# Kernel optimization log

Measured on AMD Instinct MI355X. Metric: run time of the kernel, lower is better.

Reference implementation:

```python
import jax, jax.numpy as jnp
import numpy as np

N, E = 50000, 800000          # nodes, edges
IN_DIM, HID, OUT = 200, 256, 64  # hidden_dims
R = 2                          # num_relations
NEG_SLOPE = 0.2                # RGATConv default negative_slope
EPS = 1e-16                    # PyG softmax denominator eps


def _glorot(key, shape, fan):
    return jax.random.normal(key, shape, dtype=jnp.float32) / np.float32(np.sqrt(fan))


def setup_inputs() -> dict:
    key = jax.random.key(0)
    ks = jax.random.split(key, 13)
    features = jax.random.normal(ks[0], (N, IN_DIM), dtype=jnp.float32)
    edge_index = jax.random.randint(ks[1], (2, E), 0, N, dtype=jnp.int64)
    edge_type = jax.random.randint(ks[2], (E,), 0, R, dtype=jnp.int64)
    return {
        "features": features,
        "edge_index": edge_index,
        "edge_type": edge_type,
        # RGATConv layer 1 (heads=1, dim=1): weight [R, in, out], q/k [out, 1]
        "w1": _glorot(ks[3], (R, IN_DIM, HID), IN_DIM),
        "q1": _glorot(ks[4], (HID, 1), HID),
        "k1": _glorot(ks[5], (HID, 1), HID),
        # RGATConv layer 2
        "w2": _glorot(ks[6], (R, HID, OUT), HID),
        "q2": _glorot(ks[7], (OUT, 1), OUT),
        "k2": _glorot(ks[8], (OUT, 1), OUT),
        # decoder: Linear(OUT->HID) then Linear(HID->IN_DIM), stored as [in, out]
        "dW1": _glorot(ks[9], (OUT, HID), OUT),
        "db1": jnp.zeros((HID,), jnp.float32),
        "dW2": _glorot(ks[10], (HID, IN_DIM), HID),
        "db2": jnp.zeros((IN_DIM,), jnp.float32),
    }


def rgat_conv(x, src, dst, etype, w, q, k):
    """PyG RGATConv: additive-self-attention, across-relation softmax,
    heads=1, dim=1, concat=False, bias=False, aggr=add (eval mode: no dropout)."""
    n = x.shape[0]
    # relation-specific transform at node level (per-edge bmm factors through nodes)
    xw = jnp.einsum('ni,ric->rnc', x, w)          # [R, N, C]
    qn = jnp.einsum('rnc,ch->rnh', xw, q)         # [R, N, 1]
    kn = jnp.einsum('rnc,ch->rnh', xw, k)         # [R, N, 1]
    # per-edge attention logit: leaky_relu(q_i + k_j)
    alpha = jax.nn.leaky_relu(qn[etype, dst] + kn[etype, src], NEG_SLOPE)  # [E, 1]
    # segment softmax over destination nodes (across relations)
    m = jax.lax.stop_gradient(jax.ops.segment_max(alpha, dst, num_segments=n))
    m = jnp.where(jnp.isfinite(m), m, jnp.float32(0.0))
    ea = jnp.exp(alpha - m[dst])
    denom = jax.ops.segment_sum(ea, dst, num_segments=n)
    att = ea / (denom[dst] + EPS)                 # [E, 1]
    # scatter-add weighted messages
    msg = att * xw[etype, src]                    # [E, C]
    return jax.ops.segment_sum(msg, dst, num_segments=n)  # [N, C]


def reference(features, edge_index, edge_type, w1, q1, k1, w2, q2, k2, dW1, db1, dW2, db2):
    src, dst = edge_index[0], edge_index[1]
    h1 = jax.nn.elu(rgat_conv(features, src, dst, edge_type, w1, q1, k1))
    h2 = jax.nn.elu(rgat_conv(h1, src, dst, edge_type, w2, q2, k2))
    h3 = (h2 @ dW1 + db1) @ dW2 + db2   # decoder (PCA mode: no ReLU)
    return (h2, h3)
```

## Files before the change

kernel.cpp:

```cpp
#include <hip/hip_runtime.h>

#define IN_DIM 200
#define HID    256
#define OUT_D  64
#define RREL   2
#define NEG_SLOPE 0.2f
#define NNODE  50000
#define MPAD   50048

typedef __attribute__((ext_vector_type(8))) short bf16x8;
typedef __attribute__((ext_vector_type(4))) float f32x4;
typedef __attribute__((ext_vector_type(4))) unsigned int u32x4;

__device__ __forceinline__ float bf2f(unsigned short u) {
    union { unsigned int i; float f; } v; v.i = ((unsigned int)u) << 16; return v.f;
}
__device__ __forceinline__ unsigned short f2bf(float f) {
    union { float f; unsigned int i; } v; v.f = f;
    unsigned int u = v.i;
    return (unsigned short)((u + 0x7FFFu + ((u >> 16) & 1u)) >> 16);
}
__device__ __forceinline__ float elu(float v) { return v > 0.f ? v : (__expf(v) - 1.0f); }

__global__ void feat_cvt(const float* __restrict__ in, unsigned short* __restrict__ out, int n)
{
    int t = blockIdx.x * 256 + threadIdx.x;
    int row = t / 50, c4 = (t % 50) * 4;
    if (row >= n) return;
    float4 f = *(const float4*)(in + (long long)row * 200 + c4);
    *(ushort4*)(out + (long long)row * 200 + c4) =
        make_ushort4(f2bf(f.x), f2bf(f.y), f2bf(f.z), f2bf(f.w));
}

__global__ void wt_cvt(const float* __restrict__ in, unsigned short* __restrict__ out,
                       int Kreal, int Nreal, int Kpad, int Npad, int nb)
{
    long long total = (long long)nb * Npad * Kpad;
    long long idx = (long long)blockIdx.x * 256 + threadIdx.x;
    if (idx >= total) return;
    int kk = (int)(idx % Kpad);
    long long t = idx / Kpad;
    int nrow = (int)(t % Npad);
    int z = (int)(t / Npad);
    float f = (kk < Kreal && nrow < Nreal) ? in[((long long)z * Kreal + kk) * Nreal + nrow] : 0.f;
    out[idx] = f2bf(f);
}

__global__ void wt_cvt_stack(const float* __restrict__ in, unsigned short* __restrict__ out)
{
    int idx = blockIdx.x * 256 + threadIdx.x;
    if (idx >= 2 * 256 * 256) return;
    int kk = idx & 255;
    int c  = (idx >> 8) & 255;
    int z  = idx >> 16;
    float f = (kk < IN_DIM) ? in[((long long)z * IN_DIM + kk) * 256 + c] : 0.f;
    out[(long long)c * 512 + z * 256 + kk] = f2bf(f);
}

__global__ __launch_bounds__(256) void wqk_cvt(
    const float* __restrict__ w, const float* __restrict__ q,
    const float* __restrict__ k, float* __restrict__ wqv, float* __restrict__ wkv)
{
    int wv = ((blockIdx.x << 8) + threadIdx.x) >> 6;
    int lane = threadIdx.x & 63;
    if (wv >= 512) return;
    int r = wv >> 8, kk = wv & 255;
    float sq = 0.f, sk = 0.f;
    if (kk < IN_DIM) {
        const float* row = w + ((long long)(r * IN_DIM + kk)) * 256;
        float4 wv4 = *(const float4*)(row + lane * 4);
        float4 qv4 = *(const float4*)(q + lane * 4);
        float4 kv4 = *(const float4*)(k + lane * 4);
        sq = wv4.x * qv4.x + wv4.y * qv4.y + wv4.z * qv4.z + wv4.w * qv4.w;
        sk = wv4.x * kv4.x + wv4.y * kv4.y + wv4.z * kv4.z + wv4.w * kv4.w;
        #pragma unroll
        for (int off = 32; off; off >>= 1) {
            sq += __shfl_xor(sq, off);
            sk += __shfl_xor(sk, off);
        }
    }
    if (lane == 0) { wqv[r * 256 + kk] = sq; wkv[r * 256 + kk] = sk; }
}

__global__ __launch_bounds__(256) void qk_feat(
    const unsigned short* __restrict__ A1c, const float* __restrict__ wqv,
    const float* __restrict__ wkv, float* __restrict__ qn, float* __restrict__ kn, int n)
{
    int wv = ((blockIdx.x << 8) + threadIdx.x) >> 6;
    int lane = threadIdx.x & 63;
    if (wv >= n) return;
    float x0 = 0.f, x1 = 0.f, x2 = 0.f, x3 = 0.f;
    if (lane < 50) {
        ushort4 v = *(const ushort4*)(A1c + (long long)wv * 200 + lane * 4);
        x0 = bf2f(v.x); x1 = bf2f(v.y); x2 = bf2f(v.z); x3 = bf2f(v.w);
    }
    float4 q0v = *(const float4*)(wqv + lane * 4);
    float4 k0v = *(const float4*)(wkv + lane * 4);
    float4 q1v = *(const float4*)(wqv + 256 + lane * 4);
    float4 k1v = *(const float4*)(wkv + 256 + lane * 4);
    float sq0 = x0 * q0v.x + x1 * q0v.y + x2 * q0v.z + x3 * q0v.w;
    float sk0 = x0 * k0v.x + x1 * k0v.y + x2 * k0v.z + x3 * k0v.w;
    float sq1 = x0 * q1v.x + x1 * q1v.y + x2 * q1v.z + x3 * q1v.w;
    float sk1 = x0 * k1v.x + x1 * k1v.y + x2 * k1v.z + x3 * k1v.w;
    #pragma unroll
    for (int off = 32; off; off >>= 1) {
        sq0 += __shfl_xor(sq0, off);
        sk0 += __shfl_xor(sk0, off);
        sq1 += __shfl_xor(sq1, off);
        sk1 += __shfl_xor(sk1, off);
    }
    if (lane == 0) {
        qn[wv] = sq0; qn[n + wv] = sq1;
        kn[wv] = sk0; kn[n + wv] = sk1;
    }
}

template<bool OUT_BF16, bool DO_ELU>
__global__ __launch_bounds__(256) void gemm_mfma(
    const unsigned short* __restrict__ A,
    const unsigned short* __restrict__ Bt,
    const float* __restrict__ bias,
    void* __restrict__ Cout,
    int M, int Nn, int Kp, int Npad,
    long long strideC)
{
    __shared__ __align__(16) char lds[49152];
    const int tid  = threadIdx.x;
    const int lane = tid & 63;
    const int w    = tid >> 6;
    const int m0   = blockIdx.x * 128;
    const int n0   = blockIdx.y * 64;
    const int z    = blockIdx.z;

    const char* Ab = (const char*)A;
    const char* Bb = (const char*)(Bt + (long long)z * Npad * Kp);
    const int rs = Kp * 2;

    f32x4 acc[2][4];
    #pragma unroll
    for (int i = 0; i < 2; ++i)
        #pragma unroll
        for (int j = 0; j < 4; ++j) acc[i][j] = (f32x4){0.f, 0.f, 0.f, 0.f};

    const int KT = Kp >> 6;

    auto stage = [&](int buf, int kt) {
        char* lA = lds + buf * 24576;
        char* lB = lA + 16384;
        #pragma unroll
        for (int i = 0; i < 4; ++i) {
            int g = i * 256 + tid;
            int row = g >> 3, c = g & 7;
            const char* src = Ab + (long long)(m0 + row) * rs + kt * 128 + ((c ^ (row & 7)) << 4);
            __builtin_amdgcn_global_load_lds((const __attribute__((address_space(1))) void*)src,
                                             (__attribute__((address_space(3))) void*)(lA + g * 16),
                                             16, 0, 0);
        }
        #pragma unroll
        for (int i = 0; i < 2; ++i) {
            int g = i * 256 + tid;
            int row = g >> 3, c = g & 7;
            const char* src = Bb + (long long)(n0 + row) * rs + kt * 128 + ((c ^ (row & 7)) << 4);
            __builtin_amdgcn_global_load_lds((const __attribute__((address_space(1))) void*)src,
                                             (__attribute__((address_space(3))) void*)(lB + g * 16),
                                             16, 0, 0);
        }
    };

    stage(0, 0);
    int cur = 0;
    for (int kt = 0; kt < KT; ++kt) {
        __syncthreads();
        if (kt + 1 < KT) stage(cur ^ 1, kt + 1);
        const char* lA = lds + cur * 24576;
        const char* lB = lA + 16384;
        #pragma unroll
        for (int ks = 0; ks < 2; ++ks) {
            const int kg = ks * 4 + (lane >> 4);
            bf16x8 a[2], b[4];
            #pragma unroll
            for (int mi = 0; mi < 2; ++mi) {
                int row = w * 32 + mi * 16 + (lane & 15);
                a[mi] = *(const bf16x8*)(lA + row * 128 + ((kg ^ (row & 7)) << 4));
            }
            #pragma unroll
            for (int nj = 0; nj < 4; ++nj) {
                int row = nj * 16 + (lane & 15);
                b[nj] = *(const bf16x8*)(lB + row * 128 + ((kg ^ (row & 7)) << 4));
            }
            #pragma unroll
            for (int mi = 0; mi < 2; ++mi)
                #pragma unroll
                for (int nj = 0; nj < 4; ++nj)
                    acc[mi][nj] = __builtin_amdgcn_mfma_f32_16x16x32_bf16(a[mi], b[nj], acc[mi][nj], 0, 0, 0);
        }
        cur ^= 1;
    }

    const int colb = n0 + (lane & 15);
    #pragma unroll
    for (int mi = 0; mi < 2; ++mi) {
        #pragma unroll
        for (int nj = 0; nj < 4; ++nj) {
            int col = colb + nj * 16;
            if (col >= Nn) continue;
            float badd = bias ? bias[col] : 0.f;
            #pragma unroll
            for (int r = 0; r < 4; ++r) {
                int rowm = m0 + w * 32 + mi * 16 + ((lane >> 4) << 2) + r;
                if (rowm >= M) continue;
                float v = acc[mi][nj][r] + badd;
                if (DO_ELU) v = v > 0.f ? v : (__expf(v) - 1.0f);
                if (OUT_BF16)
                    ((unsigned short*)Cout)[strideC * z + (long long)rowm * Nn + col] = f2bf(v);
                else
                    ((float*)Cout)[strideC * z + (long long)rowm * Nn + col] = v;
            }
        }
    }
}

template<int C>
__global__ __launch_bounds__(256) void qk_bf16(
    const unsigned short* __restrict__ xw, const float* __restrict__ q,
    const float* __restrict__ k, float* __restrict__ qn, float* __restrict__ kn, int n)
{
    int wv = ((blockIdx.x << 8) + threadIdx.x) >> 6;
    int lane = threadIdx.x & 63;
    if (wv >= 2 * n) return;
    int r = wv >= n;
    int node = wv - r * n;
    const unsigned short* row = xw + ((long long)r * MPAD + node) * C;
    float sq, sk;
    if (C == 256) {
        ushort4 v = *(const ushort4*)(row + lane * 4);
        float4 qv = *(const float4*)(q + lane * 4);
        float4 kv = *(const float4*)(k + lane * 4);
        float x0 = bf2f(v.x), x1 = bf2f(v.y), x2 = bf2f(v.z), x3 = bf2f(v.w);
        sq = x0 * qv.x + x1 * qv.y + x2 * qv.z + x3 * qv.w;
        sk = x0 * kv.x + x1 * kv.y + x2 * kv.z + x3 * kv.w;
    } else {
        float x = bf2f(row[lane]);
        sq = x * q[lane];
        sk = x * k[lane];
    }
    #pragma unroll
    for (int off = 32; off; off >>= 1) {
        sq += __shfl_xor(sq, off);
        sk += __shfl_xor(sk, off);
    }
    if (lane == 0) { qn[wv] = sq; kn[wv] = sk; }
}

__global__ void count_kernel(const int* __restrict__ dst, const int* __restrict__ etype,
                             int* __restrict__ deg2, int E)
{
    int e = blockIdx.x * 256 + threadIdx.x;
    if (e < E) atomicAdd(&deg2[(dst[e] << 1) | etype[e]], 1);
}

__global__ __launch_bounds__(256) void scan_blocksum(
    const int* __restrict__ deg, int* __restrict__ bsum, int n)
{
    __shared__ int red[256];
    int i = blockIdx.x * 256 + threadIdx.x;
    int v = (i < n) ? deg[i] : 0;
    red[threadIdx.x] = v;
    __syncthreads();
    #pragma unroll
    for (int off = 128; off; off >>= 1) {
        if (threadIdx.x < off) red[threadIdx.x] += red[threadIdx.x + off];
        __syncthreads();
    }
    if (threadIdx.x == 0) bsum[blockIdx.x] = red[0];
}

__global__ __launch_bounds__(512) void scan_bsum(int* __restrict__ bsum, int nb)
{
    __shared__ int buf[512];
    const int t = threadIdx.x;
    int v = (t < nb) ? bsum[t] : 0;
    buf[t] = v;
    __syncthreads();
    #pragma unroll
    for (int off = 1; off < 512; off <<= 1) {
        int u = (t >= off) ? buf[t - off] : 0;
        __syncthreads();
        buf[t] += u;
        __syncthreads();
    }
    if (t < nb) bsum[t] = buf[t] - v;
}

__global__ __launch_bounds__(256) void scan_final(
    const int* __restrict__ deg, const int* __restrict__ bsum,
    int* __restrict__ row_ptr, int* __restrict__ cursor, int n)
{
    __shared__ int buf[256];
    const int t = threadIdx.x;
    const int i = blockIdx.x * 256 + t;
    int v = (i < n) ? deg[i] : 0;
    buf[t] = v;
    __syncthreads();
    #pragma unroll
    for (int off = 1; off < 256; off <<= 1) {
        int u = (t >= off) ? buf[t - off] : 0;
        __syncthreads();
        buf[t] += u;
        __syncthreads();
    }
    int excl = bsum[blockIdx.x] + buf[t] - v;
    if (i < n) { row_ptr[i] = excl; cursor[i] = excl; }
    if (i == n - 1) row_ptr[n] = excl + v;
}

__global__ void scatter_kernel(const int* __restrict__ dst, const int* __restrict__ src,
                               const int* __restrict__ etype, int* __restrict__ cursor2,
                               int* __restrict__ epk, int E)
{
    int e = blockIdx.x * 256 + threadIdx.x;
    if (e < E) {
        int p = atomicAdd(&cursor2[(dst[e] << 1) | etype[e]], 1);
        epk[p] = src[e];
    }
}

__global__ __launch_bounds__(256) void aggregate_z(
    const unsigned short* __restrict__ A1c,
    const float* __restrict__ qn,
    const float* __restrict__ kn,
    const int* __restrict__ row_ptr2,
    const int* __restrict__ epk,
    unsigned short* __restrict__ z,
    int n)
{
    const int wv   = ((blockIdx.x << 8) + threadIdx.x) >> 6;
    const int lane = threadIdx.x & 63;
    if (wv >= n) return;
    const int d = wv;
    const int start = row_ptr2[2 * d];
    const int mid   = row_ptr2[2 * d + 1];
    const int end   = row_ptr2[2 * d + 2];
    const int cnt = end - start;
    const int c0  = mid - start;
    const float q0 = qn[d];
    const float q1 = qn[n + d];
    const int slot = lane >> 5;
    const int hl   = lane & 31;

    if (cnt <= 64) {
        int pv = 0; float a = -INFINITY;
        if (lane < cnt) {
            pv = epk[start + lane];
            bool r1 = lane >= c0;
            a = (r1 ? q1 : q0) + kn[(r1 ? n : 0) + pv];
            a = a > 0.f ? a : NEG_SLOPE * a;
        }
        float mx = a;
        #pragma unroll
        for (int off = 32; off; off >>= 1) mx = fmaxf(mx, __shfl_xor(mx, off));
        float ev = (lane < cnt) ? __expf(a - mx) : 0.f;
        float se = ev;
        #pragma unroll
        for (int off = 32; off; off >>= 1) se += __shfl_xor(se, off);
        const float wvv = ev * (1.f / (se + 1e-16f));

        #pragma unroll
        for (int seg = 0; seg < 2; ++seg) {
            const int segoff = seg ? c0 : 0;
            const int cs = seg ? (cnt - c0) : c0;
            float accA[8], accB[8];
            #pragma unroll
            for (int i = 0; i < 8; ++i) { accA[i] = 0.f; accB[i] = 0.f; }

            const int iters = (cs + 1) >> 1;
            int k = 0;
            for (; k + 2 <= iters; k += 2) {
                const int e0 = slot + k * 2;
                const int e1 = e0 + 2;
                int   pA = __shfl(pv, segoff + e0);
                float wA = __shfl(wvv, segoff + e0);
                int   pB = __shfl(pv, segoff + e1);
                float wB = __shfl(wvv, segoff + e1);
                if (e0 >= cs) wA = 0.f;
                if (e1 >= cs) wB = 0.f;
                const u32x4 rA = *(const u32x4*)(A1c + (long long)pA * 200 + hl * 8);
                const u32x4 rB = *(const u32x4*)(A1c + (long long)pB * 200 + hl * 8);
                #pragma unroll
                for (int t2 = 0; t2 < 4; ++t2) {
                    unsigned dA = rA[t2], dB = rB[t2];
                    accA[2 * t2]     = fmaf(wA, __uint_as_float(dA << 16),         accA[2 * t2]);
                    accA[2 * t2 + 1] = fmaf(wA, __uint_as_float(dA & 0xFFFF0000u), accA[2 * t2 + 1]);
                    accB[2 * t2]     = fmaf(wB, __uint_as_float(dB << 16),         accB[2 * t2]);
                    accB[2 * t2 + 1] = fmaf(wB, __uint_as_float(dB & 0xFFFF0000u), accB[2 * t2 + 1]);
                }
            }
            if (k < iters) {
                const int e0 = slot + k * 2;
                int   pA = __shfl(pv, segoff + e0);
                float wA = __shfl(wvv, segoff + e0);
                if (e0 >= cs) wA = 0.f;
                const u32x4 rA = *(const u32x4*)(A1c + (long long)pA * 200 + hl * 8);
                #pragma unroll
                for (int t2 = 0; t2 < 4; ++t2) {
                    unsigned dA = rA[t2];
                    accA[2 * t2]     = fmaf(wA, __uint_as_float(dA << 16),         accA[2 * t2]);
                    accA[2 * t2 + 1] = fmaf(wA, __uint_as_float(dA & 0xFFFF0000u), accA[2 * t2 + 1]);
                }
            }

            float acc[8];
            #pragma unroll
            for (int i = 0; i < 8; ++i) acc[i] = accA[i] + accB[i];
            #pragma unroll
            for (int t2 = 0; t2 < 8; ++t2) acc[t2] += __shfl_xor(acc[t2], 32);
            if (slot == 0) {
                u32x4 pack;
                #pragma unroll
                for (int t2 = 0; t2 < 4; ++t2)
                    pack[t2] = (unsigned)f2bf(acc[2 * t2]) | ((unsigned)f2bf(acc[2 * t2 + 1]) << 16);
                *(u32x4*)(z + (long long)d * 512 + seg * 256 + hl * 8) = pack;
            }
        }
        return;
    }

    float mx = -INFINITY;
    for (int j = start + lane; j < end; j += 64) {
        int s = epk[j];
        bool r1 = j >= mid;
        float a = (r1 ? q1 : q0) + kn[(r1 ? n : 0) + s];
        a = a > 0.f ? a : NEG_SLOPE * a;
        mx = fmaxf(mx, a);
    }
    #pragma unroll
    for (int off = 32; off; off >>= 1) mx = fmaxf(mx, __shfl_xor(mx, off));

    float se = 0.f;
    for (int j = start + lane; j < end; j += 64) {
        int s = epk[j];
        bool r1 = j >= mid;
        float a = (r1 ? q1 : q0) + kn[(r1 ? n : 0) + s];
        a = a > 0.f ? a : NEG_SLOPE * a;
        se += __expf(a - mx);
    }
    #pragma unroll
    for (int off = 32; off; off >>= 1) se += __shfl_xor(se, off);
    const float inv = 1.f / (se + 1e-16f);

    #pragma unroll
    for (int seg = 0; seg < 2; ++seg) {
        const int s0 = seg ? mid : start;
        const int s1 = seg ? end : mid;
        const float qr = seg ? q1 : q0;
        const int kbase = seg ? n : 0;

        float accA[8], accB[8];
        #pragma unroll
        for (int i = 0; i < 8; ++i) { accA[i] = 0.f; accB[i] = 0.f; }

        for (int base = s0; base < s1; base += 64) {
            const int cnt2 = min(64, s1 - base);
            int pv = 0; float wvv = 0.f;
            if (lane < cnt2) {
                pv = epk[base + lane];
                float a = qr + kn[kbase + pv];
                a = a > 0.f ? a : NEG_SLOPE * a;
                wvv = __expf(a - mx) * inv;
            }
            const int iters = (cnt2 + 1) >> 1;
            int k = 0;
            for (; k + 2 <= iters; k += 2) {
                const int e0 = slot + k * 2;
                const int e1 = e0 + 2;
                int   pA = __shfl(pv, e0);
                float wA = __shfl(wvv, e0);
                int   pB = __shfl(pv, e1);
                float wB = __shfl(wvv, e1);
                const u32x4 rA = *(const u32x4*)(A1c + (long long)pA * 200 + hl * 8);
                const u32x4 rB = *(const u32x4*)(A1c + (long long)pB * 200 + hl * 8);
                #pragma unroll
                for (int t2 = 0; t2 < 4; ++t2) {
                    unsigned dA = rA[t2], dB = rB[t2];
                    accA[2 * t2]     = fmaf(wA, __uint_as_float(dA << 16),         accA[2 * t2]);
                    accA[2 * t2 + 1] = fmaf(wA, __uint_as_float(dA & 0xFFFF0000u), accA[2 * t2 + 1]);
                    accB[2 * t2]     = fmaf(wB, __uint_as_float(dB << 16),         accB[2 * t2]);
                    accB[2 * t2 + 1] = fmaf(wB, __uint_as_float(dB & 0xFFFF0000u), accB[2 * t2 + 1]);
                }
            }
            if (k < iters) {
                const int e0 = slot + k * 2;
                int   pA = __shfl(pv, e0);
                float wA = __shfl(wvv, e0);
                const u32x4 rA = *(const u32x4*)(A1c + (long long)pA * 200 + hl * 8);
                #pragma unroll
                for (int t2 = 0; t2 < 4; ++t2) {
                    unsigned dA = rA[t2];
                    accA[2 * t2]     = fmaf(wA, __uint_as_float(dA << 16),         accA[2 * t2]);
                    accA[2 * t2 + 1] = fmaf(wA, __uint_as_float(dA & 0xFFFF0000u), accA[2 * t2 + 1]);
                }
            }
        }

        float acc[8];
        #pragma unroll
        for (int i = 0; i < 8; ++i) acc[i] = accA[i] + accB[i];
        #pragma unroll
        for (int t2 = 0; t2 < 8; ++t2) acc[t2] += __shfl_xor(acc[t2], 32);

        if (slot == 0) {
            u32x4 pack;
            #pragma unroll
            for (int t2 = 0; t2 < 4; ++t2)
                pack[t2] = (unsigned)f2bf(acc[2 * t2]) | ((unsigned)f2bf(acc[2 * t2 + 1]) << 16);
            *(u32x4*)(z + (long long)d * 512 + seg * 256 + hl * 8) = pack;
        }
    }
}

__global__ __launch_bounds__(256) void aggregate2(
    const unsigned short* __restrict__ xw,
    const float* __restrict__ qn,
    const float* __restrict__ kn,
    const int* __restrict__ row_ptr2,
    const int* __restrict__ epk,
    unsigned short* __restrict__ outb,
    float* __restrict__ outf,
    int n)
{
    constexpr int LPE   = 8;
    constexpr int NSLOT = 8;

    const int wv   = ((blockIdx.x << 8) + threadIdx.x) >> 6;
    const int lane = threadIdx.x & 63;
    if (wv >= n) return;
    const int d = wv;
    const int start = row_ptr2[2 * d];
    const int mid   = row_ptr2[2 * d + 1];
    const int end   = row_ptr2[2 * d + 2];
    const int cnt = end - start;
    const int c0  = mid - start;
    const float q0 = qn[d];
    const float q1 = qn[n + d];
    const int slot = lane / LPE;
    const int hl   = lane % LPE;

    float accA[8], accB[8];
    #pragma unroll
    for (int i = 0; i < 8; ++i) { accA[i] = 0.f; accB[i] = 0.f; }

    if (cnt <= 64) {
        int pv = 0; float a = -INFINITY;
        if (lane < cnt) {
            pv = epk[start + lane];
            bool r1 = lane >= c0;
            a = (r1 ? q1 : q0) + kn[(r1 ? n : 0) + pv];
            a = a > 0.f ? a : NEG_SLOPE * a;
        }
        float mx = a;
        #pragma unroll
        for (int off = 32; off; off >>= 1) mx = fmaxf(mx, __shfl_xor(mx, off));
        float ev = (lane < cnt) ? __expf(a - mx) : 0.f;
        float se = ev;
        #pragma unroll
        for (int off = 32; off; off >>= 1) se += __shfl_xor(se, off);
        const float wvn = ev * (1.f / (se + 1e-16f));

        const int iters = (cnt + NSLOT - 1) / NSLOT;
        int k = 0;
        for (; k + 2 <= iters; k += 2) {
            const int e0 = slot + k * NSLOT;
            const int e1 = e0 + NSLOT;
            int   pA = __shfl(pv, e0);
            float wA = __shfl(wvn, e0);
            int   pB = __shfl(pv, e1);
            float wB = __shfl(wvn, e1);
            const long long oA = ((e0 >= c0) ? (long long)MPAD * 64 : 0) + (long long)pA * 64 + hl * 8;
            const long long oB = ((e1 >= c0) ? (long long)MPAD * 64 : 0) + (long long)pB * 64 + hl * 8;
            const u32x4 rA = *(const u32x4*)(xw + oA);
            const u32x4 rB = *(const u32x4*)(xw + oB);
            #pragma unroll
            for (int t2 = 0; t2 < 4; ++t2) {
                unsigned dA = rA[t2], dB = rB[t2];
                accA[2 * t2]     = fmaf(wA, __uint_as_float(dA << 16),         accA[2 * t2]);
                accA[2 * t2 + 1] = fmaf(wA, __uint_as_float(dA & 0xFFFF0000u), accA[2 * t2 + 1]);
                accB[2 * t2]     = fmaf(wB, __uint_as_float(dB << 16),         accB[2 * t2]);
                accB[2 * t2 + 1] = fmaf(wB, __uint_as_float(dB & 0xFFFF0000u), accB[2 * t2 + 1]);
            }
        }
        if (k < iters) {
            const int e0 = slot + k * NSLOT;
            int   pA = __shfl(pv, e0);
            float wA = __shfl(wvn, e0);
            const long long oA = ((e0 >= c0) ? (long long)MPAD * 64 : 0) + (long long)pA * 64 + hl * 8;
            const u32x4 rA = *(const u32x4*)(xw + oA);
            #pragma unroll
            for (int t2 = 0; t2 < 4; ++t2) {
                unsigned dA = rA[t2];
                accA[2 * t2]     = fmaf(wA, __uint_as_float(dA << 16),         accA[2 * t2]);
                accA[2 * t2 + 1] = fmaf(wA, __uint_as_float(dA & 0xFFFF0000u), accA[2 * t2 + 1]);
            }
        }
    } else {
        float mx = -INFINITY;
        for (int j = start + lane; j < end; j += 64) {
            int s = epk[j];
            bool r1 = j >= mid;
            float a = (r1 ? q1 : q0) + kn[(r1 ? n : 0) + s];
            a = a > 0.f ? a : NEG_SLOPE * a;
            mx = fmaxf(mx, a);
        }
        #pragma unroll
        for (int off = 32; off; off >>= 1) mx = fmaxf(mx, __shfl_xor(mx, off));

        float se = 0.f;
        for (int j = start + lane; j < end; j += 64) {
            int s = epk[j];
            bool r1 = j >= mid;
            float a = (r1 ? q1 : q0) + kn[(r1 ? n : 0) + s];
            a = a > 0.f ? a : NEG_SLOPE * a;
            se += __expf(a - mx);
        }
        #pragma unroll
        for (int off = 32; off; off >>= 1) se += __shfl_xor(se, off);
        const float inv = 1.f / (se + 1e-16f);

        for (int base = start; base < end; base += 64) {
            const int cnt2 = min(64, end - base);
            int pv = 0; float wvn = 0.f;
            if (lane < cnt2) {
                int j = base + lane;
                pv = epk[j];
                bool r1 = j >= mid;
                float a = (r1 ? q1 : q0) + kn[(r1 ? n : 0) + pv];
                a = a > 0.f ? a : NEG_SLOPE * a;
                wvn = __expf(a - mx) * inv;
            }
            const int iters = (cnt2 + NSLOT - 1) / NSLOT;
            int k = 0;
            for (; k + 2 <= iters; k += 2) {
                const int e0 = slot + k * NSLOT;
                const int e1 = e0 + NSLOT;
                int   pA = __shfl(pv, e0);
                float wA = __shfl(wvn, e0);
                int   pB = __shfl(pv, e1);
                float wB = __shfl(wvn, e1);
                const long long oA = ((base + e0 >= mid) ? (long long)MPAD * 64 : 0) + (long long)pA * 64 + hl * 8;
                const long long oB = ((base + e1 >= mid) ? (long long)MPAD * 64 : 0) + (long long)pB * 64 + hl * 8;
                const u32x4 rA = *(const u32x4*)(xw + oA);
                const u32x4 rB = *(const u32x4*)(xw + oB);
                #pragma unroll
                for (int t2 = 0; t2 < 4; ++t2) {
                    unsigned dA = rA[t2], dB = rB[t2];
                    accA[2 * t2]     = fmaf(wA, __uint_as_float(dA << 16),         accA[2 * t2]);
                    accA[2 * t2 + 1] = fmaf(wA, __uint_as_float(dA & 0xFFFF0000u), accA[2 * t2 + 1]);
                    accB[2 * t2]     = fmaf(wB, __uint_as_float(dB << 16),         accB[2 * t2]);
                    accB[2 * t2 + 1] = fmaf(wB, __uint_as_float(dB & 0xFFFF0000u), accB[2 * t2 + 1]);
                }
            }
            if (k < iters) {
                const int e0 = slot + k * NSLOT;
                int   pA = __shfl(pv, e0);
                float wA = __shfl(wvn, e0);
                const long long oA = ((base + e0 >= mid) ? (long long)MPAD * 64 : 0) + (long long)pA * 64 + hl * 8;
                const u32x4 rA = *(const u32x4*)(xw + oA);
                #pragma unroll
                for (int t2 = 0; t2 < 4; ++t2) {
                    unsigned dA = rA[t2];
                    accA[2 * t2]     = fmaf(wA, __uint_as_float(dA << 16),         accA[2 * t2]);
                    accA[2 * t2 + 1] = fmaf(wA, __uint_as_float(dA & 0xFFFF0000u), accA[2 * t2 + 1]);
                }
            }
        }
    }

    float acc[8];
    #pragma unroll
    for (int i = 0; i < 8; ++i) acc[i] = accA[i] + accB[i];
    #pragma unroll
    for (int off = LPE; off < 64; off <<= 1)
        #pragma unroll
        for (int t2 = 0; t2 < 8; ++t2) acc[t2] += __shfl_xor(acc[t2], off);

    if (slot == 0) {
        float fo[8];
        #pragma unroll
        for (int t2 = 0; t2 < 8; ++t2) fo[t2] = elu(acc[t2]);
        u32x4 pack;
        #pragma unroll
        for (int t2 = 0; t2 < 4; ++t2)
            pack[t2] = (unsigned)f2bf(fo[2 * t2]) | ((unsigned)f2bf(fo[2 * t2 + 1]) << 16);
        *(u32x4*)(outb + (long long)d * 64 + hl * 8) = pack;
        *(float4*)(outf + (long long)d * 64 + hl * 8)     = make_float4(fo[0], fo[1], fo[2], fo[3]);
        *(float4*)(outf + (long long)d * 64 + hl * 8 + 4) = make_float4(fo[4], fo[5], fo[6], fo[7]);
    }
}

extern "C" void kernel_launch(void* const* d_in, const int* in_sizes, int n_in,
                              void* d_out, int out_size, void* d_ws, size_t ws_size,
                              hipStream_t stream)
{
    const float* features = (const float*)d_in[0];
    const int*   ei       = (const int*)d_in[1];
    const int*   etype    = (const int*)d_in[2];
    const float* w1       = (const float*)d_in[3];
    const float* q1       = (const float*)d_in[4];
    const float* k1       = (const float*)d_in[5];
    const float* w2       = (const float*)d_in[6];
    const float* q2       = (const float*)d_in[7];
    const float* k2       = (const float*)d_in[8];
    const float* dW1      = (const float*)d_in[9];
    const float* db1      = (const float*)d_in[10];
    const float* dW2      = (const float*)d_in[11];
    const float* db2      = (const float*)d_in[12];

    const int n = in_sizes[0] / IN_DIM;
    const int E = in_sizes[2];
    const int n2 = 2 * n;
    const int* src = ei;
    const int* dst = ei + E;

    float* out_h2 = (float*)d_out;
    float* out_h3 = out_h2 + (long long)n * OUT_D;

    char* wp = (char*)d_ws;
    auto carve = [&](size_t bytes) {
        char* p = wp; wp += (bytes + 255) & ~(size_t)255; return p;
    };
    unsigned short* A1c  = (unsigned short*)carve((size_t)n * 200 * 2 + 256);
    unsigned short* zbuf = (unsigned short*)carve((size_t)MPAD * 512 * 2);
    unsigned short* h1   = (unsigned short*)carve((size_t)MPAD * 256 * 2);
    unsigned short* xw2  = (unsigned short*)carve((size_t)2 * MPAD * 64 * 2);
    unsigned short* h2b  = (unsigned short*)carve((size_t)MPAD * 64 * 2);
    unsigned short* tdec = (unsigned short*)carve((size_t)MPAD * 256 * 2);
    unsigned short* wst  = (unsigned short*)carve((size_t)256 * 512 * 2);
    unsigned short* w2t  = (unsigned short*)carve((size_t)2 * 64 * 256 * 2);
    unsigned short* dW1t = (unsigned short*)carve((size_t)256 * 64 * 2);
    unsigned short* dW2t = (unsigned short*)carve((size_t)256 * 256 * 2);
    float* wqv    = (float*)carve((size_t)2 * 256 * 4);
    float* wkv    = (float*)carve((size_t)2 * 256 * 4);
    float* qnb    = (float*)carve((size_t)n2 * 4);
    float* knb    = (float*)carve((size_t)n2 * 4);
    int* row_ptr2 = (int*)carve((size_t)(n2 + 1) * 4);
    int* cursor2  = (int*)carve((size_t)n2 * 4);
    int* deg2     = (int*)carve((size_t)n2 * 4);
    int* bsum     = (int*)carve((size_t)512 * 4);
    int* epk      = (int*)carve((size_t)E * 4);

    const int EB  = (E + 255) / 256;
    const int NB2 = (n2 + 255) / 256;
    const int MB  = (n + 127) / 128;
    const int WAVE_N  = (n + 3) / 4;

    hipMemsetAsync(deg2, 0, (size_t)n2 * sizeof(int), stream);
    count_kernel<<<EB, 256, 0, stream>>>(dst, etype, deg2, E);
    scan_blocksum<<<NB2, 256, 0, stream>>>(deg2, bsum, n2);
    scan_bsum<<<1, 512, 0, stream>>>(bsum, NB2);
    scan_final<<<NB2, 256, 0, stream>>>(deg2, bsum, row_ptr2, cursor2, n2);
    scatter_kernel<<<EB, 256, 0, stream>>>(dst, src, etype, cursor2, epk, E);

    feat_cvt<<<(n * 50 + 255) / 256, 256, 0, stream>>>(features, A1c, n);
    wt_cvt_stack<<<(2 * 256 * 256 + 255) / 256, 256, 0, stream>>>(w1, wst);
    wt_cvt<<<(2 * 64 * 256 + 255) / 256, 256, 0, stream>>>(w2, w2t, HID, OUT_D, 256, 64, RREL);
    wt_cvt<<<(256 * 64 + 255) / 256, 256, 0, stream>>>(dW1, dW1t, OUT_D, HID, 64, 256, 1);
    wt_cvt<<<(256 * 256 + 255) / 256, 256, 0, stream>>>(dW2, dW2t, HID, IN_DIM, 256, 256, 1);
    wqk_cvt<<<128, 256, 0, stream>>>(w1, q1, k1, wqv, wkv);

    qk_feat<<<WAVE_N, 256, 0, stream>>>(A1c, wqv, wkv, qnb, knb, n);
    aggregate_z<<<WAVE_N, 256, 0, stream>>>(A1c, qnb, knb, row_ptr2, epk, zbuf, n);
    {
        dim3 g(MB, 4, 1);
        gemm_mfma<true, true><<<g, 256, 0, stream>>>(zbuf, wst, nullptr, h1,
                                                     n, HID, 512, 256, 0);
    }

    {
        dim3 g(MB, 1, RREL);
        gemm_mfma<true, false><<<g, 256, 0, stream>>>(h1, w2t, nullptr, xw2,
                                                      n, OUT_D, 256, 64, (long long)MPAD * OUT_D);
    }
    qk_bf16<OUT_D><<<(n2 + 3) / 4, 256, 0, stream>>>(xw2, q2, k2, qnb, knb, n);
    aggregate2<<<WAVE_N, 256, 0, stream>>>(xw2, qnb, knb, row_ptr2, epk,
                                           h2b, out_h2, n);

    {
        dim3 g(MB, 4, 1);
        gemm_mfma<true, false><<<g, 256, 0, stream>>>(h2b, dW1t, db1, tdec,
                                                      n, HID, 64, 256, 0);
    }
    {
        dim3 g(MB, 4, 1);
        gemm_mfma<false, false><<<g, 256, 0, stream>>>(tdec, dW2t, db2, out_h3,
                                                       n, IN_DIM, 256, 256, 0);
    }
}
```

Before: 360.3 us.

## Pad features to 256 columns, fuse layer-2 q/k into GEMM, unroll gathers

```diff
diff --git a/kernel.cpp b/kernel.cpp
--- a/kernel.cpp
+++ b/kernel.cpp
@@ -22,14 +22,20 @@
 }
 __device__ __forceinline__ float elu(float v) { return v > 0.f ? v : (__expf(v) - 1.0f); }
 
-__global__ void feat_cvt(const float* __restrict__ in, unsigned short* __restrict__ out, int n)
-{
-    int t = blockIdx.x * 256 + threadIdx.x;
-    int row = t / 50, c4 = (t % 50) * 4;
-    if (row >= n) return;
-    float4 f = *(const float4*)(in + (long long)row * 200 + c4);
-    *(ushort4*)(out + (long long)row * 200 + c4) =
-        make_ushort4(f2bf(f.x), f2bf(f.y), f2bf(f.z), f2bf(f.w));
+__global__ void feat_cvt(const float* __restrict__ in, unsigned short* __restrict__ out)
+{
+    long long idx = (long long)blockIdx.x * 256 + threadIdx.x;
+    int row = (int)(idx >> 6);
+    int c4  = ((int)idx & 63) << 2;
+    if (row >= MPAD) return;
+    unsigned short v[4];
+    #pragma unroll
+    for (int i = 0; i < 4; ++i) {
+        int c = c4 + i;
+        float f = (row < NNODE && c < IN_DIM) ? in[(long long)row * IN_DIM + c] : 0.f;
+        v[i] = f2bf(f);
+    }
+    *(ushort4*)(out + (long long)row * 256 + c4) = make_ushort4(v[0], v[1], v[2], v[3]);
 }
 
 __global__ void wt_cvt(const float* __restrict__ in, unsigned short* __restrict__ out,
@@ -83,17 +89,14 @@
 }
 
 __global__ __launch_bounds__(256) void qk_feat(
-    const unsigned short* __restrict__ A1c, const float* __restrict__ wqv,
+    const unsigned short* __restrict__ A1, const float* __restrict__ wqv,
     const float* __restrict__ wkv, float* __restrict__ qn, float* __restrict__ kn, int n)
 {
     int wv = ((blockIdx.x << 8) + threadIdx.x) >> 6;
     int lane = threadIdx.x & 63;
     if (wv >= n) return;
-    float x0 = 0.f, x1 = 0.f, x2 = 0.f, x3 = 0.f;
-    if (lane < 50) {
-        ushort4 v = *(const ushort4*)(A1c + (long long)wv * 200 + lane * 4);
-        x0 = bf2f(v.x); x1 = bf2f(v.y); x2 = bf2f(v.z); x3 = bf2f(v.w);
-    }
+    ushort4 v = *(const ushort4*)(A1 + (long long)wv * 256 + lane * 4);
+    float x0 = bf2f(v.x), x1 = bf2f(v.y), x2 = bf2f(v.z), x3 = bf2f(v.w);
     float4 q0v = *(const float4*)(wqv + lane * 4);
     float4 k0v = *(const float4*)(wkv + lane * 4);
     float4 q1v = *(const float4*)(wqv + 256 + lane * 4);
@@ -115,12 +118,14 @@
     }
 }
 
-template<bool OUT_BF16, bool DO_ELU>
+template<bool OUT_BF16, bool DO_ELU, bool FUSE_QK>
 __global__ __launch_bounds__(256) void gemm_mfma(
     const unsigned short* __restrict__ A,
     const unsigned short* __restrict__ Bt,
     const float* __restrict__ bias,
     void* __restrict__ Cout,
+    const float* __restrict__ qvec, const float* __restrict__ kvec,
+    float* __restrict__ qn_out, float* __restrict__ kn_out,
     int M, int Nn, int Kp, int Npad,
     long long strideC)
 {
@@ -218,38 +223,41 @@
             }
         }
     }
-}
-
-template<int C>
-__global__ __launch_bounds__(256) void qk_bf16(
-    const unsigned short* __restrict__ xw, const float* __restrict__ q,
-    const float* __restrict__ k, float* __restrict__ qn, float* __restrict__ kn, int n)
-{
-    int wv = ((blockIdx.x << 8) + threadIdx.x) >> 6;
-    int lane = threadIdx.x & 63;
-    if (wv >= 2 * n) return;
-    int r = wv >= n;
-    int node = wv - r * n;
-    const unsigned short* row = xw + ((long long)r * MPAD + node) * C;
-    float sq, sk;
-    if (C == 256) {
-        ushort4 v = *(const ushort4*)(row + lane * 4);
-        float4 qv = *(const float4*)(q + lane * 4);
-        float4 kv = *(const float4*)(k + lane * 4);
-        float x0 = bf2f(v.x), x1 = bf2f(v.y), x2 = bf2f(v.z), x3 = bf2f(v.w);
-        sq = x0 * qv.x + x1 * qv.y + x2 * qv.z + x3 * qv.w;
-        sk = x0 * kv.x + x1 * kv.y + x2 * kv.z + x3 * kv.w;
-    } else {
-        float x = bf2f(row[lane]);
-        sq = x * q[lane];
-        sk = x * k[lane];
-    }
-    #pragma unroll
-    for (int off = 32; off; off >>= 1) {
-        sq += __shfl_xor(sq, off);
-        sk += __shfl_xor(sk, off);
-    }
-    if (lane == 0) { qn[wv] = sq; kn[wv] = sk; }
+
+    if (FUSE_QK) {
+        float qv[4], kv[4];
+        #pragma unroll
+        for (int nj = 0; nj < 4; ++nj) {
+            int col = colb + nj * 16;
+            bool ok = col < Nn;
+            qv[nj] = ok ? qvec[col] : 0.f;
+            kv[nj] = ok ? kvec[col] : 0.f;
+        }
+        #pragma unroll
+        for (int mi = 0; mi < 2; ++mi) {
+            #pragma unroll
+            for (int r = 0; r < 4; ++r) {
+                float sq = 0.f, sk = 0.f;
+                #pragma unroll
+                for (int nj = 0; nj < 4; ++nj) {
+                    sq = fmaf(acc[mi][nj][r], qv[nj], sq);
+                    sk = fmaf(acc[mi][nj][r], kv[nj], sk);
+                }
+                #pragma unroll
+                for (int off = 1; off < 16; off <<= 1) {
+                    sq += __shfl_xor(sq, off);
+                    sk += __shfl_xor(sk, off);
+                }
+                if ((lane & 15) == 0) {
+                    int rowm = m0 + w * 32 + mi * 16 + ((lane >> 4) << 2) + r;
+                    if (rowm < M) {
+                        atomicAdd(qn_out + (long long)z * M + rowm, sq);
+                        atomicAdd(kn_out + (long long)z * M + rowm, sk);
+                    }
+                }
+            }
+        }
+    }
 }
 
 __global__ void count_kernel(const int* __restrict__ dst, const int* __restrict__ etype,
@@ -326,7 +334,7 @@
 }
 
 __global__ __launch_bounds__(256) void aggregate_z(
-    const unsigned short* __restrict__ A1c,
+    const unsigned short* __restrict__ A1,
     const float* __restrict__ qn,
     const float* __restrict__ kn,
     const int* __restrict__ row_ptr2,
@@ -348,6 +356,15 @@
     const int slot = lane >> 5;
     const int hl   = lane & 31;
 
+    auto fma8 = [](float acc[8], float w, const u32x4& r) {
+        #pragma unroll
+        for (int t2 = 0; t2 < 4; ++t2) {
+            unsigned dw = r[t2];
+            acc[2 * t2]     = fmaf(w, __uint_as_float(dw << 16),         acc[2 * t2]);
+            acc[2 * t2 + 1] = fmaf(w, __uint_as_float(dw & 0xFFFF0000u), acc[2 * t2 + 1]);
+        }
+    };
+
     if (cnt <= 64) {
         int pv = 0; float a = -INFINITY;
         if (lane < cnt) {
@@ -375,38 +392,36 @@
 
             const int iters = (cs + 1) >> 1;
             int k = 0;
-            for (; k + 2 <= iters; k += 2) {
+            for (; k + 4 <= iters; k += 4) {
+                const int e0 = slot + k * 2, e1 = e0 + 2, e2 = e0 + 4, e3 = e0 + 6;
+                int   p0 = __shfl(pv, segoff + e0);
+                float w0 = __shfl(wvv, segoff + e0);
+                int   p1 = __shfl(pv, segoff + e1);
+                float w1 = __shfl(wvv, segoff + e1);
+                int   p2 = __shfl(pv, segoff + e2);
+                float w2 = __shfl(wvv, segoff + e2);
+                int   p3 = __shfl(pv, segoff + e3);
+                float w3 = __shfl(wvv, segoff + e3);
+                if (e0 >= cs) w0 = 0.f;
+                if (e1 >= cs) w1 = 0.f;
+                if (e2 >= cs) w2 = 0.f;
+                if (e3 >= cs) w3 = 0.f;
+                const u32x4 r0 = *(const u32x4*)(A1 + (long long)p0 * 256 + hl * 8);
+                const u32x4 r1 = *(const u32x4*)(A1 + (long long)p1 * 256 + hl * 8);
+                const u32x4 r2 = *(const u32x4*)(A1 + (long long)p2 * 256 + hl * 8);
+                const u32x4 r3 = *(const u32x4*)(A1 + (long long)p3 * 256 + hl * 8);
+                fma8(accA, w0, r0);
+                fma8(accB, w1, r1);
+                fma8(accA, w2, r2);
+                fma8(accB, w3, r3);
+            }
+            for (; k < iters; ++k) {
                 const int e0 = slot + k * 2;
-                const int e1 = e0 + 2;
-                int   pA = __shfl(pv, segoff + e0);
-                float wA = __shfl(wvv, segoff + e0);
-                int   pB = __shfl(pv, segoff + e1);
-                float wB = __shfl(wvv, segoff + e1);
-                if (e0 >= cs) wA = 0.f;
-                if (e1 >= cs) wB = 0.f;
-                const u32x4 rA = *(const u32x4*)(A1c + (long long)pA * 200 + hl * 8);
-                const u32x4 rB = *(const u32x4*)(A1c + (long long)pB * 200 + hl * 8);
-                #pragma unroll
-                for (int t2 = 0; t2 < 4; ++t2) {
-                    unsigned dA = rA[t2], dB = rB[t2];
-                    accA[2 * t2]     = fmaf(wA, __uint_as_float(dA << 16),         accA[2 * t2]);
-                    accA[2 * t2 + 1] = fmaf(wA, __uint_as_float(dA & 0xFFFF0000u), accA[2 * t2 + 1]);
-                    accB[2 * t2]     = fmaf(wB, __uint_as_float(dB << 16),         accB[2 * t2]);
-                    accB[2 * t2 + 1] = fmaf(wB, __uint_as_float(dB & 0xFFFF0000u), accB[2 * t2 + 1]);
-                }
-            }
-            if (k < iters) {
-                const int e0 = slot + k * 2;
-                int   pA = __shfl(pv, segoff + e0);
-                float wA = __shfl(wvv, segoff + e0);
-                if (e0 >= cs) wA = 0.f;
-                const u32x4 rA = *(const u32x4*)(A1c + (long long)pA * 200 + hl * 8);
-                #pragma unroll
-                for (int t2 = 0; t2 < 4; ++t2) {
-                    unsigned dA = rA[t2];
-                    accA[2 * t2]     = fmaf(wA, __uint_as_float(dA << 16),         accA[2 * t2]);
-                    accA[2 * t2 + 1] = fmaf(wA, __uint_as_float(dA & 0xFFFF0000u), accA[2 * t2 + 1]);
-                }
+                int   p0 = __shfl(pv, segoff + e0);
+                float w0 = __shfl(wvv, segoff + e0);
+                if (e0 >= cs) w0 = 0.f;
+                const u32x4 r0 = *(const u32x4*)(A1 + (long long)p0 * 256 + hl * 8);
+                fma8(accA, w0, r0);
             }
 
             float acc[8];
@@ -477,28 +492,17 @@
                 float wA = __shfl(wvv, e0);
                 int   pB = __shfl(pv, e1);
                 float wB = __shfl(wvv, e1);
-                const u32x4 rA = *(const u32x4*)(A1c + (long long)pA * 200 + hl * 8);
-                const u32x4 rB = *(const u32x4*)(A1c + (long long)pB * 200 + hl * 8);
-                #pragma unroll
-                for (int t2 = 0; t2 < 4; ++t2) {
-                    unsigned dA = rA[t2], dB = rB[t2];
-                    accA[2 * t2]     = fmaf(wA, __uint_as_float(dA << 16),         accA[2 * t2]);
-                    accA[2 * t2 + 1] = fmaf(wA, __uint_as_float(dA & 0xFFFF0000u), accA[2 * t2 + 1]);
-                    accB[2 * t2]     = fmaf(wB, __uint_as_float(dB << 16),         accB[2 * t2]);
-                    accB[2 * t2 + 1] = fmaf(wB, __uint_as_float(dB & 0xFFFF0000u), accB[2 * t2 + 1]);
-                }
+                const u32x4 rA = *(const u32x4*)(A1 + (long long)pA * 256 + hl * 8);
+                const u32x4 rB = *(const u32x4*)(A1 + (long long)pB * 256 + hl * 8);
+                fma8(accA, wA, rA);
+                fma8(accB, wB, rB);
             }
             if (k < iters) {
                 const int e0 = slot + k * 2;
                 int   pA = __shfl(pv, e0);
                 float wA = __shfl(wvv, e0);
-                const u32x4 rA = *(const u32x4*)(A1c + (long long)pA * 200 + hl * 8);
-                #pragma unroll
-                for (int t2 = 0; t2 < 4; ++t2) {
-                    unsigned dA = rA[t2];
-                    accA[2 * t2]     = fmaf(wA, __uint_as_float(dA << 16),         accA[2 * t2]);
-                    accA[2 * t2 + 1] = fmaf(wA, __uint_as_float(dA & 0xFFFF0000u), accA[2 * t2 + 1]);
-                }
+                const u32x4 rA = *(const u32x4*)(A1 + (long long)pA * 256 + hl * 8);
+                fma8(accA, wA, rA);
             }
         }
 
@@ -545,6 +549,15 @@
     const int slot = lane / LPE;
     const int hl   = lane % LPE;
 
+    auto fma8 = [](float acc[8], float w, const u32x4& r) {
+        #pragma unroll
+        for (int t2 = 0; t2 < 4; ++t2) {
+            unsigned dw = r[t2];
+            acc[2 * t2]     = fmaf(w, __uint_as_float(dw << 16),         acc[2 * t2]);
+            acc[2 * t2 + 1] = fmaf(w, __uint_as_float(dw & 0xFFFF0000u), acc[2 * t2 + 1]);
+        }
+    };
+
     float accA[8], accB[8];
     #pragma unroll
     for (int i = 0; i < 8; ++i) { accA[i] = 0.f; accB[i] = 0.f; }
@@ -579,14 +592,8 @@
             const long long oB = ((e1 >= c0) ? (long long)MPAD * 64 : 0) + (long long)pB * 64 + hl * 8;
             const u32x4 rA = *(const u32x4*)(xw + oA);
             const u32x4 rB = *(const u32x4*)(xw + oB);
-            #pragma unroll
-            for (int t2 = 0; t2 < 4; ++t2) {
-                unsigned dA = rA[t2], dB = rB[t2];
-                accA[2 * t2]     = fmaf(wA, __uint_as_float(dA << 16),         accA[2 * t2]);
-                accA[2 * t2 + 1] = fmaf(wA, __uint_as_float(dA & 0xFFFF0000u), accA[2 * t2 + 1]);
-                accB[2 * t2]     = fmaf(wB, __uint_as_float(dB << 16),         accB[2 * t2]);
-                accB[2 * t2 + 1] = fmaf(wB, __uint_as_float(dB & 0xFFFF0000u), accB[2 * t2 + 1]);
-            }
+            fma8(accA, wA, rA);
+            fma8(accB, wB, rB);
         }
         if (k < iters) {
             const int e0 = slot + k * NSLOT;
@@ -594,12 +601,7 @@
             float wA = __shfl(wvn, e0);
             const long long oA = ((e0 >= c0) ? (long long)MPAD * 64 : 0) + (long long)pA * 64 + hl * 8;
             const u32x4 rA = *(const u32x4*)(xw + oA);
-            #pragma unroll
-            for (int t2 = 0; t2 < 4; ++t2) {
-                unsigned dA = rA[t2];
-                accA[2 * t2]     = fmaf(wA, __uint_as_float(dA << 16),         accA[2 * t2]);
-                accA[2 * t2 + 1] = fmaf(wA, __uint_as_float(dA & 0xFFFF0000u), accA[2 * t2 + 1]);
-            }
+            fma8(accA, wA, rA);
         }
     } else {
         float mx = -INFINITY;
@@ -649,14 +651,8 @@
                 const long long oB = ((base + e1 >= mid) ? (long long)MPAD * 64 : 0) + (long long)pB * 64 + hl * 8;
                 const u32x4 rA = *(const u32x4*)(xw + oA);
                 const u32x4 rB = *(const u32x4*)(xw + oB);
-                #pragma unroll
-                for (int t2 = 0; t2 < 4; ++t2) {
-                    unsigned dA = rA[t2], dB = rB[t2];
-                    accA[2 * t2]     = fmaf(wA, __uint_as_float(dA << 16),         accA[2 * t2]);
-                    accA[2 * t2 + 1] = fmaf(wA, __uint_as_float(dA & 0xFFFF0000u), accA[2 * t2 + 1]);
-                    accB[2 * t2]     = fmaf(wB, __uint_as_float(dB << 16),         accB[2 * t2]);
-                    accB[2 * t2 + 1] = fmaf(wB, __uint_as_float(dB & 0xFFFF0000u), accB[2 * t2 + 1]);
-                }
+                fma8(accA, wA, rA);
+                fma8(accB, wB, rB);
             }
             if (k < iters) {
                 const int e0 = slot + k * NSLOT;
@@ -664,12 +660,7 @@
                 float wA = __shfl(wvn, e0);
                 const long long oA = ((base + e0 >= mid) ? (long long)MPAD * 64 : 0) + (long long)pA * 64 + hl * 8;
                 const u32x4 rA = *(const u32x4*)(xw + oA);
-                #pragma unroll
-                for (int t2 = 0; t2 < 4; ++t2) {
-                    unsigned dA = rA[t2];
-                    accA[2 * t2]     = fmaf(wA, __uint_as_float(dA << 16),         accA[2 * t2]);
-                    accA[2 * t2 + 1] = fmaf(wA, __uint_as_float(dA & 0xFFFF0000u), accA[2 * t2 + 1]);
-                }
+                fma8(accA, wA, rA);
             }
         }
     }
@@ -727,7 +718,7 @@
     auto carve = [&](size_t bytes) {
         char* p = wp; wp += (bytes + 255) & ~(size_t)255; return p;
     };
-    unsigned short* A1c  = (unsigned short*)carve((size_t)n * 200 * 2 + 256);
+    unsigned short* A1   = (unsigned short*)carve((size_t)MPAD * 256 * 2);
     unsigned short* zbuf = (unsigned short*)carve((size_t)MPAD * 512 * 2);
     unsigned short* h1   = (unsigned short*)carve((size_t)MPAD * 256 * 2);
     unsigned short* xw2  = (unsigned short*)carve((size_t)2 * MPAD * 64 * 2);
@@ -759,38 +750,43 @@
     scan_final<<<NB2, 256, 0, stream>>>(deg2, bsum, row_ptr2, cursor2, n2);
     scatter_kernel<<<EB, 256, 0, stream>>>(dst, src, etype, cursor2, epk, E);
 
-    feat_cvt<<<(n * 50 + 255) / 256, 256, 0, stream>>>(features, A1c, n);
+    feat_cvt<<<(MPAD * 64 + 255) / 256, 256, 0, stream>>>(features, A1);
     wt_cvt_stack<<<(2 * 256 * 256 + 255) / 256, 256, 0, stream>>>(w1, wst);
     wt_cvt<<<(2 * 64 * 256 + 255) / 256, 256, 0, stream>>>(w2, w2t, HID, OUT_D, 256, 64, RREL);
     wt_cvt<<<(256 * 64 + 255) / 256, 256, 0, stream>>>(dW1, dW1t, OUT_D, HID, 64, 256, 1);
     wt_cvt<<<(256 * 256 + 255) / 256, 256, 0, stream>>>(dW2, dW2t, HID, IN_DIM, 256, 256, 1);
     wqk_cvt<<<128, 256, 0, stream>>>(w1, q1, k1, wqv, wkv);
 
-    qk_feat<<<WAVE_N, 256, 0, stream>>>(A1c, wqv, wkv, qnb, knb, n);
-    aggregate_z<<<WAVE_N, 256, 0, stream>>>(A1c, qnb, knb, row_ptr2, epk, zbuf, n);
+    qk_feat<<<WAVE_N, 256, 0, stream>>>(A1, wqv, wkv, qnb, knb, n);
+    aggregate_z<<<WAVE_N, 256, 0, stream>>>(A1, qnb, knb, row_ptr2, epk, zbuf, n);
     {
         dim3 g(MB, 4, 1);
-        gemm_mfma<true, true><<<g, 256, 0, stream>>>(zbuf, wst, nullptr, h1,
-                                                     n, HID, 512, 256, 0);
-    }
-
+        gemm_mfma<true, true, false><<<g, 256, 0, stream>>>(zbuf, wst, nullptr, h1,
+                                                            nullptr, nullptr, nullptr, nullptr,
+                                                            n, HID, 512, 256, 0);
+    }
+
+    hipMemsetAsync(qnb, 0, (size_t)n2 * 4, stream);
+    hipMemsetAsync(knb, 0, (size_t)n2 * 4, stream);
     {
         dim3 g(MB, 1, RREL);
-        gemm_mfma<true, false><<<g, 256, 0, stream>>>(h1, w2t, nullptr, xw2,
-                                                      n, OUT_D, 256, 64, (long long)MPAD * OUT_D);
-    }
-    qk_bf16<OUT_D><<<(n2 + 3) / 4, 256, 0, stream>>>(xw2, q2, k2, qnb, knb, n);
+        gemm_mfma<true, false, true><<<g, 256, 0, stream>>>(h1, w2t, nullptr, xw2,
+                                                            q2, k2, qnb, knb,
+                                                            n, OUT_D, 256, 64, (long long)MPAD * OUT_D);
+    }
     aggregate2<<<WAVE_N, 256, 0, stream>>>(xw2, qnb, knb, row_ptr2, epk,
                                            h2b, out_h2, n);
 
     {
         dim3 g(MB, 4, 1);
-        gemm_mfma<true, false><<<g, 256, 0, stream>>>(h2b, dW1t, db1, tdec,
-                                                      n, HID, 64, 256, 0);
+        gemm_mfma<true, false, false><<<g, 256, 0, stream>>>(h2b, dW1t, db1, tdec,
+                                                             nullptr, nullptr, nullptr, nullptr,
+                                                             n, HID, 64, 256, 0);
     }
     {
         dim3 g(MB, 4, 1);
-        gemm_mfma<false, false><<<g, 256, 0, stream>>>(tdec, dW2t, db2, out_h3,
-                                                       n, IN_DIM, 256, 256, 0);
-    }
-}
+        gemm_mfma<false, false, false><<<g, 256, 0, stream>>>(tdec, dW2t, db2, out_h3,
+                                                              nullptr, nullptr, nullptr, nullptr,
+                                                              n, IN_DIM, 256, 256, 0);
+    }
+}
```

Result: faster. 351.4 us (-2.5%).
